# Kernel optimization log

Hardware: AMD Instinct MI355X
Metric: run time of the kernel (lower is better)

## Reference

```python
import jax, jax.numpy as jnp
import numpy as np

H = 2048       # hidden_size
E = 8          # num_experts
K = 2          # top_k
I = 16         # expert bottleneck (intermediate_size)


def setup_inputs() -> dict:
    key = jax.random.key(0)
    k1, k2, k3, k4 = jax.random.split(key, 4)
    B, T = 2, 4096
    x = jax.random.normal(k1, (B, T, H), dtype=jnp.float32)
    # nn.Linear weight layout is (out, in); init scale ~ 1/sqrt(fan_in)
    router_w = jax.random.normal(k2, (E, H), dtype=jnp.float32) / np.sqrt(H)
    down_w = jax.random.normal(k3, (E, I, H), dtype=jnp.float32) / np.sqrt(H)
    up_w = jax.random.normal(k4, (E, H, I), dtype=jnp.float32) / np.sqrt(I)
    return {"x": x, "router_w": router_w, "down_w": down_w, "up_w": up_w}


def reference(x, router_w, down_w, up_w):
    # router
    logits = jnp.einsum('bth,eh->bte', x, router_w)        # [B,T,E]
    weights = jax.nn.softmax(logits, axis=-1)
    top_w, top_idx = jax.lax.top_k(weights, K)             # [B,T,K]
    # gate[b,t,e] = softmax weight if e in top-k else 0 (top-k of softmax
    # values are distinct a.s., so masking == scatter of top_w)
    topk_mask = jnp.sum(jax.nn.one_hot(top_idx, E, dtype=x.dtype), axis=-2)  # [B,T,E]
    gate = weights * topk_mask                              # [B,T,E]
    # dense expert compute on all tokens (matches original's redundant compute)
    h = jnp.einsum('bth,eih->beti', x, down_w)             # [B,E,T,I]
    a = jax.nn.silu(h)
    expert_out = jnp.einsum('beti,ehi->beth', a, up_w)     # [B,E,T,H]
    # masked combine
    out = jnp.einsum('beth,bte->bth', expert_out, gate)    # [B,T,H]
    return out
```

## Files before the change

### kernel.cpp

```cpp
#include <hip/hip_runtime.h>
#include <math.h>

#define HDIM 2048
#define NEXP 8
#define IDIM 16
#define N_EI 128
#define TB   16

typedef __attribute__((ext_vector_type(8))) short bf16x8;
typedef __attribute__((ext_vector_type(4))) float f32x4;

static __device__ __forceinline__ short f2bf(float f) {
    union { float f; unsigned u; } v; v.f = f;
    unsigned r = v.u + 0x7fffu + ((v.u >> 16) & 1u);
    return (short)(r >> 16);
}

__global__ __launch_bounds__(256) void prep_kernel(
    const float* __restrict__ x, const float* __restrict__ rw,
    const float* __restrict__ dw, const float* __restrict__ uw,
    float* __restrict__ gate_ws, short* __restrict__ b1p, short* __restrict__ b2p,
    int T, int routerBlocks)
{
    const int bid = blockIdx.x;
    if (bid < routerBlocks) {
        const int wave = threadIdx.x >> 6, lane = threadIdx.x & 63;
        const int t = bid * 4 + wave;
        if (t >= T) return;
        const float* __restrict__ xr = x + (size_t)t * HDIM;
        float4 xv[8];
        #pragma unroll
        for (int j = 0; j < 8; ++j) xv[j] = *(const float4*)(xr + j * 256 + lane * 4);
        float logit[NEXP];
        #pragma unroll
        for (int e = 0; e < NEXP; ++e) {
            const float* __restrict__ wr = rw + (size_t)e * HDIM;
            float acc = 0.f;
            #pragma unroll
            for (int j = 0; j < 8; ++j) {
                float4 wv = *(const float4*)(wr + j * 256 + lane * 4);
                acc += xv[j].x * wv.x + xv[j].y * wv.y + xv[j].z * wv.z + xv[j].w * wv.w;
            }
            #pragma unroll
            for (int s = 1; s < 64; s <<= 1) acc += __shfl_xor(acc, s);
            logit[e] = acc;
        }
        if (lane == 0) {
            float m = logit[0];
            #pragma unroll
            for (int e = 1; e < NEXP; ++e) m = fmaxf(m, logit[e]);
            float w[NEXP], ssum = 0.f;
            #pragma unroll
            for (int e = 0; e < NEXP; ++e) { w[e] = expf(logit[e] - m); ssum += w[e]; }
            const float inv = 1.f / ssum;
            #pragma unroll
            for (int e = 0; e < NEXP; ++e) w[e] *= inv;
            int i1 = 0; float w1 = w[0];
            #pragma unroll
            for (int e = 1; e < NEXP; ++e) if (w[e] > w1) { w1 = w[e]; i1 = e; }
            int i2 = -1; float w2 = -1.f;
            #pragma unroll
            for (int e = 0; e < NEXP; ++e) if (e != i1 && w[e] > w2) { w2 = w[e]; i2 = e; }
            #pragma unroll
            for (int e = 0; e < NEXP; ++e)
                gate_ws[(size_t)t * NEXP + e] = (e == i1) ? w1 : ((e == i2) ? w2 : 0.f);
        }
    } else {
        const int wb = bid - routerBlocks;
        const int base = (wb * 256 + threadIdx.x) * 16;
        #pragma unroll 4
        for (int j = 0; j < 16; ++j) {
            const int d = base + j;
            {
                const int k = ((d >> 10) << 3) | (d & 7);
                const int n = (d >> 3) & 127;
                b1p[d] = f2bf(dw[(size_t)n * HDIM + k]);
            }
            {
                const int k2 = ((d >> 14) << 3) | (d & 7);
                const int h = (d >> 3) & 2047;
                b2p[d] = f2bf(uw[((size_t)(k2 >> 4) * HDIM + h) * IDIM + (k2 & 15)]);
            }
        }
    }
}

__global__ __launch_bounds__(512) void moe_mfma_kernel(
    const float* __restrict__ x, const float* __restrict__ gate_ws,
    const short* __restrict__ b1p, const short* __restrict__ b2p,
    float* __restrict__ out, int T)
{
    __shared__ float h_part[TB][N_EI];
    __shared__ short a_s[TB][N_EI];
    __shared__ float gate_s[TB][NEXP];

    const int tid = threadIdx.x;
    const int w = tid >> 6, l = tid & 63;
    const int row = l & 15, kblk = l >> 4;
    const int t0 = blockIdx.x * TB;

    if (tid < TB * NEXP)
        gate_s[tid >> 3][tid & 7] = gate_ws[(size_t)(t0 + (tid >> 3)) * NEXP + (tid & 7)];
    __syncthreads();

    const int nq = w & 3, kh = w >> 2;
    const int n0 = nq * 32;
    f32x4 acc0 = {0.f, 0.f, 0.f, 0.f}, acc1 = {0.f, 0.f, 0.f, 0.f};
    const float* __restrict__ xrow = x + (size_t)(t0 + row) * HDIM;

    for (int s = 0; s < 32; ++s) {
        const int k0 = kh * 1024 + s * 32;
        const int ka = k0 + kblk * 8;
        float4 a0 = *(const float4*)(xrow + ka);
        float4 a1 = *(const float4*)(xrow + ka + 4);
        bf16x8 af;
        af[0] = f2bf(a0.x); af[1] = f2bf(a0.y); af[2] = f2bf(a0.z); af[3] = f2bf(a0.w);
        af[4] = f2bf(a1.x); af[5] = f2bf(a1.y); af[6] = f2bf(a1.z); af[7] = f2bf(a1.w);
        const short* __restrict__ bbase = b1p + ((size_t)(k0 >> 3) + kblk) * 1024;
        bf16x8 bf0 = *(const bf16x8*)(bbase + (n0 + row) * 8);
        bf16x8 bf1 = *(const bf16x8*)(bbase + (n0 + 16 + row) * 8);
        acc0 = __builtin_amdgcn_mfma_f32_16x16x32_bf16(af, bf0, acc0, 0, 0, 0);
        acc1 = __builtin_amdgcn_mfma_f32_16x16x32_bf16(af, bf1, acc1, 0, 0, 0);
    }

    if (kh == 1) {
        #pragma unroll
        for (int r = 0; r < 4; ++r) {
            h_part[kblk * 4 + r][n0 + row]      = acc0[r];
            h_part[kblk * 4 + r][n0 + 16 + row] = acc1[r];
        }
    }
    __syncthreads();
    if (kh == 0) {
        const int e0 = nq * 2, e1 = nq * 2 + 1;
        #pragma unroll
        for (int r = 0; r < 4; ++r) {
            const int t = kblk * 4 + r;
            float hv0 = acc0[r] + h_part[t][n0 + row];
            float hv1 = acc1[r] + h_part[t][n0 + 16 + row];
            float sv0 = hv0 / (1.f + expf(-hv0)) * gate_s[t][e0];
            float sv1 = hv1 / (1.f + expf(-hv1)) * gate_s[t][e1];
            a_s[t][n0 + row]      = f2bf(sv0);
            a_s[t][n0 + 16 + row] = f2bf(sv1);
        }
    }
    __syncthreads();

    const int h0 = w * 256;
    f32x4 acc[16];
    #pragma unroll
    for (int f = 0; f < 16; ++f) acc[f] = (f32x4){0.f, 0.f, 0.f, 0.f};

    for (int s = 0; s < 4; ++s) {
        bf16x8 af = *(const bf16x8*)(&a_s[row][s * 32 + kblk * 8]);
        const short* __restrict__ bbase = b2p + ((size_t)(s * 4) + kblk) * 16384;
        #pragma unroll
        for (int f = 0; f < 16; ++f) {
            bf16x8 bfr = *(const bf16x8*)(bbase + (size_t)(h0 + f * 16 + row) * 8);
            acc[f] = __builtin_amdgcn_mfma_f32_16x16x32_bf16(af, bfr, acc[f], 0, 0, 0);
        }
    }
    #pragma unroll
    for (int f = 0; f < 16; ++f) {
        #pragma unroll
        for (int r = 0; r < 4; ++r) {
            out[(size_t)(t0 + kblk * 4 + r) * HDIM + h0 + f * 16 + row] = acc[f][r];
        }
    }
}

extern "C" void kernel_launch(void* const* d_in, const int* in_sizes, int n_in,
                              void* d_out, int out_size, void* d_ws, size_t ws_size,
                              hipStream_t stream) {
    const float* x  = (const float*)d_in[0];
    const float* rw = (const float*)d_in[1];
    const float* dw = (const float*)d_in[2];
    const float* uw = (const float*)d_in[3];
    float* out = (float*)d_out;
    const int T = in_sizes[0] / HDIM;

    float* gate_ws = (float*)d_ws;
    short* b1p = (short*)((char*)d_ws + (size_t)T * NEXP * 4);
    short* b2p = (short*)((char*)d_ws + (size_t)T * NEXP * 4 + 262144 * 2);

    const int routerBlocks = T / 4;
    prep_kernel<<<routerBlocks + 64, 256, 0, stream>>>(x, rw, dw, uw,
                                                       gate_ws, b1p, b2p, T, routerBlocks);
    moe_mfma_kernel<<<T / TB, 512, 0, stream>>>(x, gate_ws, b1p, b2p, out, T);
}
```

Baseline: 181.9 us.

## Swap MFMA operands for row-contiguous output and vectorize weight packing

Swaps the A/B operands of the MFMA calls so each lane holds four consecutive hidden columns of one token. The output can then be written as 16-byte nontemporal vector stores, and the LDS exchanges for h_part and a_s become vector accesses, with padding added to reduce bank conflicts. The weight-packing part of the prep kernel is rewritten so each thread does two float4 reads and one bf16x8 store instead of scalar gathers, which uses more blocks. The main cost targeted is the strided scalar output store of the large fp32 result.

After: 180.4 us. About the same (-0.8%).

```diff
diff --git a/kernel.cpp b/kernel.cpp
--- a/kernel.cpp
+++ b/kernel.cpp
@@ -66,22 +66,28 @@
                 gate_ws[(size_t)t * NEXP + e] = (e == i1) ? w1 : ((e == i2) ? w2 : 0.f);
         }
     } else {
-        const int wb = bid - routerBlocks;
-        const int base = (wb * 256 + threadIdx.x) * 16;
-        #pragma unroll 4
-        for (int j = 0; j < 16; ++j) {
-            const int d = base + j;
-            {
-                const int k = ((d >> 10) << 3) | (d & 7);
-                const int n = (d >> 3) & 127;
-                b1p[d] = f2bf(dw[(size_t)n * HDIM + k]);
-            }
-            {
-                const int k2 = ((d >> 14) << 3) | (d & 7);
-                const int h = (d >> 3) & 2047;
-                b2p[d] = f2bf(uw[((size_t)(k2 >> 4) * HDIM + h) * IDIM + (k2 & 15)]);
-            }
+        const int id = (bid - routerBlocks) * 256 + threadIdx.x;
+        float4 v0, v1;
+        short* dst;
+        if (id < 32768) {
+            const int kb = id >> 7, n = id & 127;
+            const float* __restrict__ src = dw + (size_t)n * HDIM + kb * 8;
+            v0 = *(const float4*)(src);
+            v1 = *(const float4*)(src + 4);
+            dst = b1p + (size_t)id * 8;
+        } else {
+            const int id2 = id - 32768;
+            const int k2b = id2 >> 11, h = id2 & 2047;
+            const int e = k2b >> 1, i0 = (k2b & 1) * 8;
+            const float* __restrict__ src = uw + ((size_t)e * HDIM + h) * IDIM + i0;
+            v0 = *(const float4*)(src);
+            v1 = *(const float4*)(src + 4);
+            dst = b2p + (size_t)id2 * 8;
         }
+        bf16x8 p;
+        p[0] = f2bf(v0.x); p[1] = f2bf(v0.y); p[2] = f2bf(v0.z); p[3] = f2bf(v0.w);
+        p[4] = f2bf(v1.x); p[5] = f2bf(v1.y); p[6] = f2bf(v1.z); p[7] = f2bf(v1.w);
+        *(bf16x8*)dst = p;
     }
 }
 
@@ -90,13 +96,14 @@
     const short* __restrict__ b1p, const short* __restrict__ b2p,
     float* __restrict__ out, int T)
 {
-    __shared__ float h_part[TB][N_EI];
-    __shared__ short a_s[TB][N_EI];
+    __shared__ float h_part[TB][132];
+    __shared__ short a_s[TB][136];
     __shared__ float gate_s[TB][NEXP];
 
     const int tid = threadIdx.x;
     const int w = tid >> 6, l = tid & 63;
-    const int row = l & 15, kblk = l >> 4;
+    const int c = l & 15;
+    const int kblk = l >> 4;
     const int t0 = blockIdx.x * TB;
 
     if (tid < TB * NEXP)
@@ -106,43 +113,45 @@
     const int nq = w & 3, kh = w >> 2;
     const int n0 = nq * 32;
     f32x4 acc0 = {0.f, 0.f, 0.f, 0.f}, acc1 = {0.f, 0.f, 0.f, 0.f};
-    const float* __restrict__ xrow = x + (size_t)(t0 + row) * HDIM;
+    const float* __restrict__ xrow = x + (size_t)(t0 + c) * HDIM;
 
     for (int s = 0; s < 32; ++s) {
         const int k0 = kh * 1024 + s * 32;
         const int ka = k0 + kblk * 8;
         float4 a0 = *(const float4*)(xrow + ka);
         float4 a1 = *(const float4*)(xrow + ka + 4);
-        bf16x8 af;
-        af[0] = f2bf(a0.x); af[1] = f2bf(a0.y); af[2] = f2bf(a0.z); af[3] = f2bf(a0.w);
-        af[4] = f2bf(a1.x); af[5] = f2bf(a1.y); af[6] = f2bf(a1.z); af[7] = f2bf(a1.w);
+        bf16x8 xf;
+        xf[0] = f2bf(a0.x); xf[1] = f2bf(a0.y); xf[2] = f2bf(a0.z); xf[3] = f2bf(a0.w);
+        xf[4] = f2bf(a1.x); xf[5] = f2bf(a1.y); xf[6] = f2bf(a1.z); xf[7] = f2bf(a1.w);
         const short* __restrict__ bbase = b1p + ((size_t)(k0 >> 3) + kblk) * 1024;
-        bf16x8 bf0 = *(const bf16x8*)(bbase + (n0 + row) * 8);
-        bf16x8 bf1 = *(const bf16x8*)(bbase + (n0 + 16 + row) * 8);
-        acc0 = __builtin_amdgcn_mfma_f32_16x16x32_bf16(af, bf0, acc0, 0, 0, 0);
-        acc1 = __builtin_amdgcn_mfma_f32_16x16x32_bf16(af, bf1, acc1, 0, 0, 0);
+        bf16x8 wf0 = *(const bf16x8*)(bbase + (n0 + c) * 8);
+        bf16x8 wf1 = *(const bf16x8*)(bbase + (n0 + 16 + c) * 8);
+        acc0 = __builtin_amdgcn_mfma_f32_16x16x32_bf16(wf0, xf, acc0, 0, 0, 0);
+        acc1 = __builtin_amdgcn_mfma_f32_16x16x32_bf16(wf1, xf, acc1, 0, 0, 0);
     }
 
     if (kh == 1) {
-        #pragma unroll
-        for (int r = 0; r < 4; ++r) {
-            h_part[kblk * 4 + r][n0 + row]      = acc0[r];
-            h_part[kblk * 4 + r][n0 + 16 + row] = acc1[r];
-        }
+        *(f32x4*)&h_part[c][n0 + kblk * 4]      = acc0;
+        *(f32x4*)&h_part[c][n0 + 16 + kblk * 4] = acc1;
     }
     __syncthreads();
     if (kh == 0) {
         const int e0 = nq * 2, e1 = nq * 2 + 1;
+        const f32x4 hp0 = *(const f32x4*)&h_part[c][n0 + kblk * 4];
+        const f32x4 hp1 = *(const f32x4*)&h_part[c][n0 + 16 + kblk * 4];
+        const float g0 = gate_s[c][e0], g1 = gate_s[c][e1];
+        short r0[4], r1[4];
         #pragma unroll
         for (int r = 0; r < 4; ++r) {
-            const int t = kblk * 4 + r;
-            float hv0 = acc0[r] + h_part[t][n0 + row];
-            float hv1 = acc1[r] + h_part[t][n0 + 16 + row];
-            float sv0 = hv0 / (1.f + expf(-hv0)) * gate_s[t][e0];
-            float sv1 = hv1 / (1.f + expf(-hv1)) * gate_s[t][e1];
-            a_s[t][n0 + row]      = f2bf(sv0);
-            a_s[t][n0 + 16 + row] = f2bf(sv1);
+            const float h0v = acc0[r] + hp0[r];
+            const float h1v = acc1[r] + hp1[r];
+            r0[r] = f2bf(h0v / (1.f + expf(-h0v)) * g0);
+            r1[r] = f2bf(h1v / (1.f + expf(-h1v)) * g1);
         }
+        *(uint2*)&a_s[c][n0 + kblk * 4]      = make_uint2(((unsigned short)r0[0]) | ((unsigned)(unsigned short)r0[1] << 16),
+                                                          ((unsigned short)r0[2]) | ((unsigned)(unsigned short)r0[3] << 16));
+        *(uint2*)&a_s[c][n0 + 16 + kblk * 4] = make_uint2(((unsigned short)r1[0]) | ((unsigned)(unsigned short)r1[1] << 16),
+                                                          ((unsigned short)r1[2]) | ((unsigned)(unsigned short)r1[3] << 16));
     }
     __syncthreads();
 
@@ -152,20 +161,18 @@
     for (int f = 0; f < 16; ++f) acc[f] = (f32x4){0.f, 0.f, 0.f, 0.f};
 
     for (int s = 0; s < 4; ++s) {
-        bf16x8 af = *(const bf16x8*)(&a_s[row][s * 32 + kblk * 8]);
+        bf16x8 af = *(const bf16x8*)(&a_s[c][s * 32 + kblk * 8]);
         const short* __restrict__ bbase = b2p + ((size_t)(s * 4) + kblk) * 16384;
         #pragma unroll
         for (int f = 0; f < 16; ++f) {
-            bf16x8 bfr = *(const bf16x8*)(bbase + (size_t)(h0 + f * 16 + row) * 8);
-            acc[f] = __builtin_amdgcn_mfma_f32_16x16x32_bf16(af, bfr, acc[f], 0, 0, 0);
+            bf16x8 wfr = *(const bf16x8*)(bbase + (size_t)(h0 + f * 16 + c) * 8);
+            acc[f] = __builtin_amdgcn_mfma_f32_16x16x32_bf16(wfr, af, acc[f], 0, 0, 0);
         }
     }
+    float* __restrict__ orow = out + (size_t)(t0 + c) * HDIM;
     #pragma unroll
     for (int f = 0; f < 16; ++f) {
-        #pragma unroll
-        for (int r = 0; r < 4; ++r) {
-            out[(size_t)(t0 + kblk * 4 + r) * HDIM + h0 + f * 16 + row] = acc[f][r];
-        }
+        __builtin_nontemporal_store(acc[f], (f32x4*)(orow + h0 + f * 16 + kblk * 4));
     }
 }
 
@@ -181,10 +188,10 @@
 
     float* gate_ws = (float*)d_ws;
     short* b1p = (short*)((char*)d_ws + (size_t)T * NEXP * 4);
-    short* b2p = (short*)((char*)d_ws + (size_t)T * NEXP * 4 + 262144 * 2);
+    short* b2p = (short*)((char*)d_ws + (size_t)T * NEXP * 4 + 524288);
 
     const int routerBlocks = T / 4;
-    prep_kernel<<<routerBlocks + 64, 256, 0, stream>>>(x, rw, dw, uw,
-                                                       gate_ws, b1p, b2p, T, routerBlocks);
+    prep_kernel<<<routerBlocks + 256, 256, 0, stream>>>(x, rw, dw, uw,
+                                                        gate_ws, b1p, b2p, T, routerBlocks);
     moe_mfma_kernel<<<T / TB, 512, 0, stream>>>(x, gate_ws, b1p, b2p, out, T);
 }
```
